# Optimization experiments

Measured on AMD Instinct MI355X. Metric: run time of the kernel, lower is better.

## Reference

```python
import jax, jax.numpy as jnp
import numpy as np

HEADS = 2

def gat_layer(x, edge_index, W, att, bias):
    # x: [N, Fin], W: [H*C, Fin], att: [1, H, 2C], bias: [C]
    N = x.shape[0]
    C = bias.shape[0]
    # add self loops (source_to_target: x_j from row 0, aggregate onto row 1)
    loop = jnp.arange(N, dtype=edge_index.dtype)
    src = jnp.concatenate([edge_index[0], loop])
    dst = jnp.concatenate([edge_index[1], loop])
    h = (x @ W.T).reshape(N, HEADS, C)          # [N, H, C]
    x_j = h[src]                                 # [E, H, C]
    x_i = h[dst]                                 # [E, H, C]
    x_cat = jnp.concatenate([x_i, x_j], axis=-1) # [E, H, 2C]
    alpha = (x_cat * att).sum(-1)                # [E, H]
    alpha = jnp.where(alpha >= 0, alpha, 0.2 * alpha)  # leaky_relu(0.2)
    # NOTE: module uses a global (not per-destination) normalization
    alpha = jnp.exp(alpha - alpha.max())
    alpha = alpha / (alpha.sum(axis=0, keepdims=True) + 1e-10)
    msg = x_j * alpha[..., None]                 # [E, H, C]
    aggr = jax.ops.segment_sum(msg, dst, num_segments=N)  # [N, H, C]
    return aggr.mean(axis=1) + bias              # [N, C]

def setup_inputs() -> dict:
    key = jax.random.key(0)
    ks = jax.random.split(key, 7)
    N, Fin, C = 50000, 128, 64
    E = 800000
    x = jax.random.normal(ks[0], (N, Fin), dtype=jnp.float32)
    edge_index = jax.random.randint(ks[1], (2, E), 0, N, dtype=jnp.int64)
    W1 = jax.random.normal(ks[2], (HEADS * C, Fin), dtype=jnp.float32) * 0.05
    att1 = jax.random.normal(ks[3], (1, HEADS, 2 * C), dtype=jnp.float32) * 0.05
    b1 = jnp.zeros((C,), dtype=jnp.float32)
    W2 = jax.random.normal(ks[4], (HEADS * C, C), dtype=jnp.float32) * 0.05
    att2 = jax.random.normal(ks[5], (1, HEADS, 2 * C), dtype=jnp.float32) * 0.05
    b2 = jnp.zeros((C,), dtype=jnp.float32)
    return {"x": x, "edge_index": edge_index, "W1": W1, "att1": att1,
            "b1": b1, "W2": W2, "att2": att2, "b2": b2}

def reference(x, edge_index, W1, att1, b1, W2, att2, b2):
    h = gat_layer(x, edge_index, W1, att1, b1)
    h = jax.nn.relu(h)
    # F.dropout with training flag: treated as eval (identity) for determinism
    out = gat_layer(h, edge_index, W2, att2, b2)
    return out
```

## Files before the change

kernel.cpp:

```cpp
#include <hip/hip_runtime.h>
#include <hip/hip_bf16.h>
#include <math.h>


#define HP 8
#define HG 64
#define NHISTB (HP * HG)
#define HRANGE_MAX 6272
#define NSELF 16
#define NWGT  256

using short8 = __attribute__((ext_vector_type(8))) short;
using f32x4  = __attribute__((ext_vector_type(4))) float;

__device__ __forceinline__ unsigned f2bf(float x) {
  unsigned u = __float_as_uint(x);
  return (u + 0x7fffu + ((u >> 16) & 1u)) >> 16;
}
__device__ __forceinline__ float bflo(unsigned p) { return __uint_as_float(p << 16); }
__device__ __forceinline__ float bfhi(unsigned p) { return __uint_as_float(p & 0xffff0000u); }
__device__ __forceinline__ float lrexp(float a) {
  a = a >= 0.f ? a : 0.2f * a;
  return __expf(a);
}

__device__ __forceinline__ void block_zadd(float z0, float z1,
                                           float* __restrict__ Zp) {
  __shared__ float r0[16], r1[16];
  int lane = threadIdx.x & 63, w = threadIdx.x >> 6;
  int nw = blockDim.x >> 6;
#pragma unroll
  for (int off = 32; off; off >>= 1) {
    z0 += __shfl_down(z0, off, 64);
    z1 += __shfl_down(z1, off, 64);
  }
  if (lane == 0) { r0[w] = z0; r1[w] = z1; }
  __syncthreads();
  if (threadIdx.x == 0) {
    float s0 = 0.f, s1 = 0.f;
    for (int i = 0; i < nw; ++i) { s0 += r0[i]; s1 += r1[i]; }
    atomicAdd(&Zp[0], s0);
    atomicAdd(&Zp[1], s1);
  }
}

__global__ __launch_bounds__(256) void init_ws(
    const float* __restrict__ W1, const float* __restrict__ W2,
    unsigned short* __restrict__ wbf1, unsigned short* __restrict__ wbf2,
    float* __restrict__ Z) {
  int tid = blockIdx.x * 256 + threadIdx.x;
  int stride = gridDim.x * 256;
  for (int i = tid; i < 128 * 128; i += stride)
    wbf1[i] = (unsigned short)f2bf(W1[i]);
  for (int i = tid; i < 128 * 64; i += stride)
    wbf2[i] = (unsigned short)f2bf(W2[i]);
  if (tid < 4) Z[tid] = 0.f;
}

template <int FIN>
__global__ __launch_bounds__(256) void gemm_mfma(
    const float* __restrict__ x, const unsigned short* __restrict__ Wb,
    const float* __restrict__ att, unsigned* __restrict__ hq,
    float* __restrict__ si, float* __restrict__ sj,
    int N,
    const int* __restrict__ dstE, unsigned short* __restrict__ partial,
    int E, int nhistb, int hstep, int eper) {
  const int tid = threadIdx.x;

  constexpr int WB = 128 * FIN * 2;
  constexpr int SMEM = (WB > HRANGE_MAX * 4) ? WB : HRANGE_MAX * 4;
  __shared__ __align__(16) unsigned char smem[SMEM];

  if ((int)blockIdx.x < nhistb) {
    int* lhist = (int*)smem;
    const int p = blockIdx.x & (HP - 1);
    const int g = blockIdx.x >> 3;
    const int lo = p * hstep;
    for (int i = tid; i < hstep; i += 256) lhist[i] = 0;
    __syncthreads();
    const int eb = g * eper;
    const int ee = min(E, eb + eper);
    int e = eb + tid;
    for (; e + 3 * 256 < ee; e += 4 * 256) {
      int d0 = dstE[e] - lo;
      int d1 = dstE[e + 256] - lo;
      int d2 = dstE[e + 2 * 256] - lo;
      int d3 = dstE[e + 3 * 256] - lo;
      if ((unsigned)d0 < (unsigned)hstep) atomicAdd(&lhist[d0], 1);
      if ((unsigned)d1 < (unsigned)hstep) atomicAdd(&lhist[d1], 1);
      if ((unsigned)d2 < (unsigned)hstep) atomicAdd(&lhist[d2], 1);
      if ((unsigned)d3 < (unsigned)hstep) atomicAdd(&lhist[d3], 1);
    }
    for (; e < ee; e += 256) {
      int d = dstE[e] - lo;
      if ((unsigned)d < (unsigned)hstep) atomicAdd(&lhist[d], 1);
    }
    __syncthreads();
    for (int i = tid; i < hstep; i += 256) {
      int node = lo + i;
      if (node < N) partial[(size_t)g * N + node] = (unsigned short)lhist[i];
    }
    return;
  }

  constexpr int KS = FIN / 32;
  constexpr int CPR = FIN / 8;
  constexpr int NCHUNK = 128 * CPR;

  unsigned short* wlds = (unsigned short*)smem;

  const int w    = tid >> 6;
  const int lane = tid & 63;
  const int cl   = lane & 15;
  const int grp  = lane >> 4;
  const int n0   = (blockIdx.x - nhistb) * 64;

  const int arow = n0 + w * 16 + cl;
  const bool avalid = arow < N;
  float4 av0[KS], av1[KS];
#pragma unroll
  for (int ks = 0; ks < KS; ++ks) {
    av0[ks] = make_float4(0.f, 0.f, 0.f, 0.f);
    av1[ks] = av0[ks];
    if (avalid) {
      const float4* xp =
          (const float4*)(x + (size_t)arow * FIN + ks * 32 + grp * 8);
      av0[ks] = xp[0];
      av1[ks] = xp[1];
    }
  }

  const uint4* Wb4 = (const uint4*)Wb;
  for (int c = tid; c < NCHUNK; c += 256) {
    int row = c / CPR;
    int cc  = c & (CPR - 1);
    *(uint4*)&wlds[row * FIN + ((cc ^ (row & (CPR - 1))) * 8)] = Wb4[c];
  }
  __syncthreads();

  short8 afrag[KS];
#pragma unroll
  for (int ks = 0; ks < KS; ++ks) {
    union { short8 s8; unsigned u[4]; } af;
    af.u[0] = f2bf(av0[ks].x) | (f2bf(av0[ks].y) << 16);
    af.u[1] = f2bf(av0[ks].z) | (f2bf(av0[ks].w) << 16);
    af.u[2] = f2bf(av1[ks].x) | (f2bf(av1[ks].y) << 16);
    af.u[3] = f2bf(av1[ks].z) | (f2bf(av1[ks].w) << 16);
    afrag[ks] = af.s8;
  }

  f32x4 acc[8];
#pragma unroll
  for (int ct = 0; ct < 8; ++ct) acc[ct] = (f32x4){0.f, 0.f, 0.f, 0.f};

  const int swz = cl & (CPR - 1);
#pragma unroll
  for (int ks = 0; ks < KS; ++ks) {
#pragma unroll
    for (int ct = 0; ct < 8; ++ct) {
      const unsigned short* bp =
          &wlds[(ct * 16 + cl) * FIN + (((ks * 4 + grp) ^ swz) * 8)];
      short8 bfrag = *(const short8*)bp;
      acc[ct] = __builtin_amdgcn_mfma_f32_16x16x32_bf16(afrag[ks], bfrag,
                                                        acc[ct], 0, 0, 0);
    }
  }

  float ai[8], aj[8];
#pragma unroll
  for (int ct = 0; ct < 8; ++ct) {
    int hd = ct >> 2;
    int cw = (ct & 3) * 16 + cl;
    ai[ct] = att[hd * 128 + cw];
    aj[ct] = att[hd * 128 + 64 + cw];
  }

#pragma unroll
  for (int r = 0; r < 4; ++r) {
    int node = n0 + w * 16 + grp * 4 + r;
    float s0i = 0.f, s0j = 0.f, s1i = 0.f, s1j = 0.f;
    unsigned wpk[4];
#pragma unroll
    for (int ct = 0; ct < 4; ++ct) {
      float v0 = acc[ct][r];
      float v1 = acc[ct + 4][r];
      s0i += v0 * ai[ct];
      s0j += v0 * aj[ct];
      s1i += v1 * ai[ct + 4];
      s1j += v1 * aj[ct + 4];
      wpk[ct] = f2bf(v0) | (f2bf(v1) << 16);
    }
#pragma unroll
    for (int off = 8; off; off >>= 1) {
      s0i += __shfl_xor(s0i, off, 64);
      s0j += __shfl_xor(s0j, off, 64);
      s1i += __shfl_xor(s1i, off, 64);
      s1j += __shfl_xor(s1j, off, 64);
    }
    if (node < N) {
#pragma unroll
      for (int ct = 0; ct < 4; ++ct)
        hq[(size_t)node * 64 + ct * 16 + cl] = wpk[ct];
      if (cl == 0) {
        si[node * 2 + 0] = s0i;
        si[node * 2 + 1] = s1i;
        sj[node * 2 + 0] = s0j;
        sj[node * 2 + 1] = s1j;
      }
    }
  }
}

__global__ __launch_bounds__(256) void scan_blocks(
    const unsigned short* __restrict__ partial, int* __restrict__ rowptr,
    int* __restrict__ bsum, int N) {
  __shared__ int ts[256];
  int b = blockIdx.x, t = threadIdx.x;
  int base = b * 1024 + t * 4;
  int s0 = 0, s1 = 0, s2 = 0, s3 = 0;
  if (base < N) {
#pragma unroll 4
    for (int g = 0; g < HG; ++g) {
      unsigned long long v =
          *(const unsigned long long*)&partial[(size_t)g * N + base];
      s0 += (int)(v & 0xffffu);
      s1 += (int)((v >> 16) & 0xffffu);
      s2 += (int)((v >> 32) & 0xffffu);
      s3 += (int)((v >> 48) & 0xffffu);
    }
  }
  int v[4] = {s0, s1, s2, s3};
  int tot = s0 + s1 + s2 + s3;
  ts[t] = tot;
  __syncthreads();
#pragma unroll
  for (int off = 1; off < 256; off <<= 1) {
    int x = (t >= off) ? ts[t - off] : 0;
    __syncthreads();
    ts[t] += x;
    __syncthreads();
  }
  int run = ts[t] - tot;
#pragma unroll
  for (int j = 0; j < 4; ++j) {
    if (base + j < N) rowptr[base + j] = run;
    run += v[j];
  }
  if (t == 255) bsum[b] = ts[255];
}

__global__ __launch_bounds__(256) void scan_finish(
    int* __restrict__ rowptr, const int* __restrict__ bsum,
    unsigned short* __restrict__ partial, int N, int Eall, int nb) {
  __shared__ int pre[256];
  if (threadIdx.x == 0) {
    int run = 0;
    for (int i = 0; i < nb; ++i) { pre[i] = run; run += bsum[i]; }
  }
  __syncthreads();
  int tid = blockIdx.x * blockDim.x + threadIdx.x;
  int stride = gridDim.x * blockDim.x;
  for (int i = tid; i < N; i += stride) {
    int v = rowptr[i] + pre[i >> 10];
    rowptr[i] = v;
    int run = 0;
#pragma unroll 8
    for (int g = 0; g < HG; ++g) {
      int c = partial[(size_t)g * N + i];
      partial[(size_t)g * N + i] = (unsigned short)run;
      run += c;
    }
  }
  if (tid == 0) rowptr[N] = Eall;
}

__global__ __launch_bounds__(1024) void scatter_z(
    const int* __restrict__ srcE, const int* __restrict__ dstE,
    const unsigned short* __restrict__ partial, const int* __restrict__ rowptr,
    float4* __restrict__ erec,
    const float2* __restrict__ si2, const float2* __restrict__ sj2,
    float* __restrict__ Zp, int E, int hstep, int N, int eper) {
  __shared__ __align__(16) int lcur[HRANGE_MAX];
  const int tid = threadIdx.x;
  float z0 = 0.f, z1 = 0.f;

  if ((int)blockIdx.x < NSELF) {
    for (int n = blockIdx.x * 1024 + tid; n < N; n += NSELF * 1024) {
      float2 a = si2[n], b = sj2[n];
      z0 += lrexp(a.x + b.x);
      z1 += lrexp(a.y + b.y);
    }
    block_zadd(z0, z1, Zp);
    return;
  }

  const int bid = blockIdx.x - NSELF;
  const int p = bid & (HP - 1);
  const int g = bid >> 3;
  const int lo = p * hstep;
  for (int i = tid; i < hstep; i += 1024) {
    int node = lo + i;
    lcur[i] = (node < N)
                  ? rowptr[node] + (int)partial[(size_t)g * N + node]
                  : 0;
  }
  __syncthreads();

  const int eb = g * eper;
  const int ee = min(E, eb + eper);
  int e = eb + tid;
  for (; e + 3 * 1024 < ee; e += 4 * 1024) {
    int d0 = dstE[e], d1 = dstE[e + 1024];
    int d2 = dstE[e + 2 * 1024], d3 = dstE[e + 3 * 1024];
    int s0 = srcE[e], s1 = srcE[e + 1024];
    int s2 = srcE[e + 2 * 1024], s3 = srcE[e + 3 * 1024];
    int t0 = d0 - lo, t1 = d1 - lo, t2 = d2 - lo, t3 = d3 - lo;
    if ((unsigned)t0 < (unsigned)hstep) {
      float2 siv = si2[d0], sjv = sj2[s0];
      float w0 = lrexp(siv.x + sjv.x), w1 = lrexp(siv.y + sjv.y);
      z0 += w0; z1 += w1;
      erec[atomicAdd(&lcur[t0], 1)] =
          make_float4(__int_as_float(s0), __int_as_float(d0), w0, w1);
    }
    if ((unsigned)t1 < (unsigned)hstep) {
      float2 siv = si2[d1], sjv = sj2[s1];
      float w0 = lrexp(siv.x + sjv.x), w1 = lrexp(siv.y + sjv.y);
      z0 += w0; z1 += w1;
      erec[atomicAdd(&lcur[t1], 1)] =
          make_float4(__int_as_float(s1), __int_as_float(d1), w0, w1);
    }
    if ((unsigned)t2 < (unsigned)hstep) {
      float2 siv = si2[d2], sjv = sj2[s2];
      float w0 = lrexp(siv.x + sjv.x), w1 = lrexp(siv.y + sjv.y);
      z0 += w0; z1 += w1;
      erec[atomicAdd(&lcur[t2], 1)] =
          make_float4(__int_as_float(s2), __int_as_float(d2), w0, w1);
    }
    if ((unsigned)t3 < (unsigned)hstep) {
      float2 siv = si2[d3], sjv = sj2[s3];
      float w0 = lrexp(siv.x + sjv.x), w1 = lrexp(siv.y + sjv.y);
      z0 += w0; z1 += w1;
      erec[atomicAdd(&lcur[t3], 1)] =
          make_float4(__int_as_float(s3), __int_as_float(d3), w0, w1);
    }
  }
  for (; e < ee; e += 1024) {
    int d = dstE[e];
    int dd = d - lo;
    if ((unsigned)dd < (unsigned)hstep) {
      int s = srcE[e];
      float2 siv = si2[d], sjv = sj2[s];
      float w0 = lrexp(siv.x + sjv.x), w1 = lrexp(siv.y + sjv.y);
      z0 += w0; z1 += w1;
      erec[atomicAdd(&lcur[dd], 1)] =
          make_float4(__int_as_float(s), __int_as_float(d), w0, w1);
    }
  }
  block_zadd(z0, z1, Zp);
}

__global__ __launch_bounds__(1024) void z_wgt2(
    const float2* __restrict__ si2, const float2* __restrict__ sj2,
    float* __restrict__ Zp, float4* __restrict__ erec, int E, int N) {
  const int tid = threadIdx.x;
  float z0 = 0.f, z1 = 0.f;
  if ((int)blockIdx.x < NSELF) {
    for (int n = blockIdx.x * 1024 + tid; n < N; n += NSELF * 1024) {
      float2 a = si2[n], b = sj2[n];
      z0 += lrexp(a.x + b.x);
      z1 += lrexp(a.y + b.y);
    }
  } else {
    int k = (blockIdx.x - NSELF) * 1024 + tid;
    for (; k < E; k += NWGT * 1024) {
      float4 r = erec[k];
      int s = __float_as_int(r.x);
      int d = __float_as_int(r.y);
      float2 siv = si2[d];
      float2 sjv = sj2[s];
      r.z = lrexp(siv.x + sjv.x);
      r.w = lrexp(siv.y + sjv.y);
      z0 += r.z; z1 += r.w;
      erec[k] = r;
    }
  }
  block_zadd(z0, z1, Zp);
}

__device__ __forceinline__ void edge8r(
    const float4* __restrict__ erec, int k, const unsigned* __restrict__ hq,
    int lane, float& acc0, float& acc1) {
  float4 r0 = erec[k],     r1 = erec[k + 1], r2 = erec[k + 2], r3 = erec[k + 3];
  float4 r4 = erec[k + 4], r5 = erec[k + 5], r6 = erec[k + 6], r7 = erec[k + 7];
  unsigned p0 = hq[(size_t)__float_as_int(r0.x) * 64 + lane];
  unsigned p1 = hq[(size_t)__float_as_int(r1.x) * 64 + lane];
  unsigned p2 = hq[(size_t)__float_as_int(r2.x) * 64 + lane];
  unsigned p3 = hq[(size_t)__float_as_int(r3.x) * 64 + lane];
  unsigned p4 = hq[(size_t)__float_as_int(r4.x) * 64 + lane];
  unsigned p5 = hq[(size_t)__float_as_int(r5.x) * 64 + lane];
  unsigned p6 = hq[(size_t)__float_as_int(r6.x) * 64 + lane];
  unsigned p7 = hq[(size_t)__float_as_int(r7.x) * 64 + lane];
  acc0 = fmaf(bflo(p0), r0.z, acc0);  acc1 = fmaf(bfhi(p0), r0.w, acc1);
  acc0 = fmaf(bflo(p1), r1.z, acc0);  acc1 = fmaf(bfhi(p1), r1.w, acc1);
  acc0 = fmaf(bflo(p2), r2.z, acc0);  acc1 = fmaf(bfhi(p2), r2.w, acc1);
  acc0 = fmaf(bflo(p3), r3.z, acc0);  acc1 = fmaf(bfhi(p3), r3.w, acc1);
  acc0 = fmaf(bflo(p4), r4.z, acc0);  acc1 = fmaf(bfhi(p4), r4.w, acc1);
  acc0 = fmaf(bflo(p5), r5.z, acc0);  acc1 = fmaf(bfhi(p5), r5.w, acc1);
  acc0 = fmaf(bflo(p6), r6.z, acc0);  acc1 = fmaf(bfhi(p6), r6.w, acc1);
  acc0 = fmaf(bflo(p7), r7.z, acc0);  acc1 = fmaf(bfhi(p7), r7.w, acc1);
}
__device__ __forceinline__ void edge4r(
    const float4* __restrict__ erec, int k, const unsigned* __restrict__ hq,
    int lane, float& acc0, float& acc1) {
  float4 r0 = erec[k], r1 = erec[k + 1], r2 = erec[k + 2], r3 = erec[k + 3];
  unsigned p0 = hq[(size_t)__float_as_int(r0.x) * 64 + lane];
  unsigned p1 = hq[(size_t)__float_as_int(r1.x) * 64 + lane];
  unsigned p2 = hq[(size_t)__float_as_int(r2.x) * 64 + lane];
  unsigned p3 = hq[(size_t)__float_as_int(r3.x) * 64 + lane];
  acc0 = fmaf(bflo(p0), r0.z, acc0);  acc1 = fmaf(bfhi(p0), r0.w, acc1);
  acc0 = fmaf(bflo(p1), r1.z, acc0);  acc1 = fmaf(bfhi(p1), r1.w, acc1);
  acc0 = fmaf(bflo(p2), r2.z, acc0);  acc1 = fmaf(bfhi(p2), r2.w, acc1);
  acc0 = fmaf(bflo(p3), r3.z, acc0);  acc1 = fmaf(bfhi(p3), r3.w, acc1);
}
__device__ __forceinline__ void edge1r(
    int s, float w0, float w1, const unsigned* __restrict__ hq, int lane,
    float& acc0, float& acc1) {
  unsigned p = hq[(size_t)s * 64 + lane];
  acc0 = fmaf(bflo(p), w0, acc0);
  acc1 = fmaf(bfhi(p), w1, acc1);
}

__global__ __launch_bounds__(256) void csr_aggregate(
    const int* __restrict__ rowptr, const float4* __restrict__ erec,
    const unsigned* __restrict__ hq, const float2* __restrict__ si2,
    const float2* __restrict__ sj2, const float* __restrict__ Zp,
    const float* __restrict__ bias, float* __restrict__ out,
    int N, int do_relu) {
  int lane = threadIdx.x & 63;
  int wid = (blockIdx.x * blockDim.x + threadIdx.x) >> 6;
  int nw = (gridDim.x * blockDim.x) >> 6;
  float z0 = 1.f / (Zp[0] + 1e-10f);
  float z1 = 1.f / (Zp[1] + 1e-10f);
  float bv = bias[lane];
  for (int n0 = wid; n0 < N; n0 += nw) {
    int n = __builtin_amdgcn_readfirstlane(n0);
    int beg = rowptr[n], end = rowptr[n + 1];
    float2 siv = si2[n];
    float2 jv = sj2[n];
    float acc0 = 0.f, acc1 = 0.f;
    edge1r(n, lrexp(siv.x + jv.x), lrexp(siv.y + jv.y), hq, lane, acc0, acc1);
    int k = beg;
    for (; k + 8 <= end; k += 8) edge8r(erec, k, hq, lane, acc0, acc1);
    if (k + 4 <= end) { edge4r(erec, k, hq, lane, acc0, acc1); k += 4; }
    for (; k < end; ++k) {
      float4 r = erec[k];
      edge1r(__float_as_int(r.x), r.z, r.w, hq, lane, acc0, acc1);
    }
    float r = 0.5f * (acc0 * z0 + acc1 * z1) + bv;
    if (do_relu) r = fmaxf(r, 0.f);
    out[(size_t)n * 64 + lane] = r;
  }
}

extern "C" void kernel_launch(void* const* d_in, const int* in_sizes, int n_in,
                              void* d_out, int out_size, void* d_ws, size_t ws_size,
                              hipStream_t stream) {
  const float* x    = (const float*)d_in[0];
  const int*   ei   = (const int*)d_in[1];
  const float* W1   = (const float*)d_in[2];
  const float* att1 = (const float*)d_in[3];
  const float* b1   = (const float*)d_in[4];
  const float* W2   = (const float*)d_in[5];
  const float* att2 = (const float*)d_in[6];
  const float* b2   = (const float*)d_in[7];
  float* out = (float*)d_out;

  const int N = in_sizes[0] / 128;
  const int E = in_sizes[1] / 2;
  const int* srcE = ei;
  const int* dstE = ei + E;

  unsigned* hq = (unsigned*)d_ws;
  float* si    = (float*)(hq + (size_t)N * 64);
  float* sj    = si + (size_t)N * 2;
  float* Z     = sj + (size_t)N * 2;
  float* x2    = Z + 4;
  unsigned short* partial = (unsigned short*)x2;
  int* rowptr  = (int*)(x2 + (size_t)N * 64);
  int* bsum    = rowptr + (N + 1);
  uintptr_t ep = ((uintptr_t)(bsum + 256) + 15) & ~(uintptr_t)15;
  float4* erec = (float4*)ep;
  unsigned short* wbf1 = (unsigned short*)(erec + E);
  unsigned short* wbf2 = wbf1 + 128 * 128;

  dim3 blk(256);
  dim3 blk1k(1024);
  int nb = (N + 1023) / 1024;
  int ntiles = (N + 63) / 64;
  int hstep = (N + HP - 1) / HP;
  int eper  = (E + HG - 1) / HG;

  init_ws<<<64, blk, 0, stream>>>(W1, W2, wbf1, wbf2, Z);
  gemm_mfma<128><<<NHISTB + ntiles, blk, 0, stream>>>(
      x, wbf1, att1, hq, si, sj, N, dstE, partial, E, NHISTB, hstep, eper);
  scan_blocks<<<nb, blk, 0, stream>>>(partial, rowptr, bsum, N);
  scan_finish<<<256, blk, 0, stream>>>(rowptr, bsum, partial, N, E, nb);
  scatter_z<<<NSELF + NHISTB, blk1k, 0, stream>>>(
      srcE, dstE, partial, rowptr, erec, (const float2*)si,
      (const float2*)sj, Z, E, hstep, N, eper);
  csr_aggregate<<<4096, blk, 0, stream>>>(rowptr, erec, hq,
                                          (const float2*)si, (const float2*)sj,
                                          Z, b1, x2, N, 1);
  gemm_mfma<64><<<ntiles, blk, 0, stream>>>(
      x2, wbf2, att2, hq, si, sj, N, dstE, partial, E, 0, hstep, eper);
  z_wgt2<<<NSELF + NWGT, blk1k, 0, stream>>>(
      (const float2*)si, (const float2*)sj, Z + 2, erec, E, N);
  csr_aggregate<<<4096, blk, 0, stream>>>(rowptr, erec, hq,
                                          (const float2*)si, (const float2*)sj,
                                          Z + 2, b2, out, N, 0);
}
```

Measured before the change: 247.9 us.

## Fuse two-pass scan into decoupled single-pass scan; store layer-1 output as bf16

Replaces the scan_blocks plus scan_finish pair with one kernel. Each block publishes its total through a flag array and spins on the flags of earlier blocks to get its prefix, and it rewrites the per-group partial offsets in the same pass. Separately, the first aggregation writes its activations as bf16, and the second GEMM loads bf16 fragments directly with no conversion. This removes a launch, a reread of partial, and half of the x2 traffic. In exchange it relies on all earlier blocks being resident for the spin-wait to make progress, and it assumes nb is at most 64 to fit the flags array.

```diff
diff --git a/kernel.cpp b/kernel.cpp
--- a/kernel.cpp
+++ b/kernel.cpp
@@ -47,7 +47,7 @@
 __global__ __launch_bounds__(256) void init_ws(
     const float* __restrict__ W1, const float* __restrict__ W2,
     unsigned short* __restrict__ wbf1, unsigned short* __restrict__ wbf2,
-    float* __restrict__ Z) {
+    float* __restrict__ Z, int* __restrict__ flags) {
   int tid = blockIdx.x * 256 + threadIdx.x;
   int stride = gridDim.x * 256;
   for (int i = tid; i < 128 * 128; i += stride)
@@ -55,11 +55,12 @@
   for (int i = tid; i < 128 * 64; i += stride)
     wbf2[i] = (unsigned short)f2bf(W2[i]);
   if (tid < 4) Z[tid] = 0.f;
-}
-
-template <int FIN>
+  if (tid < 64) flags[tid] = -1;
+}
+
+template <int FIN, bool AB16>
 __global__ __launch_bounds__(256) void gemm_mfma(
-    const float* __restrict__ x, const unsigned short* __restrict__ Wb,
+    const void* __restrict__ xin, const unsigned short* __restrict__ Wb,
     const float* __restrict__ att, unsigned* __restrict__ hq,
     float* __restrict__ si, float* __restrict__ sj,
     int N,
@@ -117,16 +118,33 @@
 
   const int arow = n0 + w * 16 + cl;
   const bool avalid = arow < N;
-  float4 av0[KS], av1[KS];
+
+  short8 afrag[KS];
 #pragma unroll
   for (int ks = 0; ks < KS; ++ks) {
-    av0[ks] = make_float4(0.f, 0.f, 0.f, 0.f);
-    av1[ks] = av0[ks];
-    if (avalid) {
-      const float4* xp =
-          (const float4*)(x + (size_t)arow * FIN + ks * 32 + grp * 8);
-      av0[ks] = xp[0];
-      av1[ks] = xp[1];
+    if constexpr (AB16) {
+      short8 z = {0, 0, 0, 0, 0, 0, 0, 0};
+      afrag[ks] = z;
+      if (avalid) {
+        const unsigned short* xb = (const unsigned short*)xin;
+        afrag[ks] =
+            *(const short8*)(xb + (size_t)arow * FIN + ks * 32 + grp * 8);
+      }
+    } else {
+      float4 v0 = make_float4(0.f, 0.f, 0.f, 0.f), v1 = v0;
+      if (avalid) {
+        const float* xf = (const float*)xin;
+        const float4* xp =
+            (const float4*)(xf + (size_t)arow * FIN + ks * 32 + grp * 8);
+        v0 = xp[0];
+        v1 = xp[1];
+      }
+      union { short8 s8; unsigned u[4]; } af;
+      af.u[0] = f2bf(v0.x) | (f2bf(v0.y) << 16);
+      af.u[1] = f2bf(v0.z) | (f2bf(v0.w) << 16);
+      af.u[2] = f2bf(v1.x) | (f2bf(v1.y) << 16);
+      af.u[3] = f2bf(v1.z) | (f2bf(v1.w) << 16);
+      afrag[ks] = af.s8;
     }
   }
 
@@ -137,17 +155,6 @@
     *(uint4*)&wlds[row * FIN + ((cc ^ (row & (CPR - 1))) * 8)] = Wb4[c];
   }
   __syncthreads();
-
-  short8 afrag[KS];
-#pragma unroll
-  for (int ks = 0; ks < KS; ++ks) {
-    union { short8 s8; unsigned u[4]; } af;
-    af.u[0] = f2bf(av0[ks].x) | (f2bf(av0[ks].y) << 16);
-    af.u[1] = f2bf(av0[ks].z) | (f2bf(av0[ks].w) << 16);
-    af.u[2] = f2bf(av1[ks].x) | (f2bf(av1[ks].y) << 16);
-    af.u[3] = f2bf(av1[ks].z) | (f2bf(av1[ks].w) << 16);
-    afrag[ks] = af.s8;
-  }
 
   f32x4 acc[8];
 #pragma unroll
@@ -211,26 +218,31 @@
   }
 }
 
-__global__ __launch_bounds__(256) void scan_blocks(
-    const unsigned short* __restrict__ partial, int* __restrict__ rowptr,
-    int* __restrict__ bsum, int N) {
+__global__ __launch_bounds__(256) void scan_full(
+    unsigned short* __restrict__ partial, int* __restrict__ rowptr,
+    int* __restrict__ flags, int N, int Eall, int nb) {
   __shared__ int ts[256];
-  int b = blockIdx.x, t = threadIdx.x;
-  int base = b * 1024 + t * 4;
-  int s0 = 0, s1 = 0, s2 = 0, s3 = 0;
+  __shared__ int pre_s;
+  const int b = blockIdx.x, t = threadIdx.x;
+  const int base = b * 1024 + t * 4;
+  int r0 = 0, r1 = 0, r2 = 0, r3 = 0;
   if (base < N) {
-#pragma unroll 4
+#pragma unroll 8
     for (int g = 0; g < HG; ++g) {
-      unsigned long long v =
-          *(const unsigned long long*)&partial[(size_t)g * N + base];
-      s0 += (int)(v & 0xffffu);
-      s1 += (int)((v >> 16) & 0xffffu);
-      s2 += (int)((v >> 32) & 0xffffu);
-      s3 += (int)((v >> 48) & 0xffffu);
-    }
-  }
-  int v[4] = {s0, s1, s2, s3};
-  int tot = s0 + s1 + s2 + s3;
+      unsigned long long* p =
+          (unsigned long long*)&partial[(size_t)g * N + base];
+      unsigned long long v = *p;
+      *p = (unsigned long long)(unsigned short)r0 |
+           ((unsigned long long)(unsigned short)r1 << 16) |
+           ((unsigned long long)(unsigned short)r2 << 32) |
+           ((unsigned long long)(unsigned short)r3 << 48);
+      r0 += (int)(v & 0xffffu);
+      r1 += (int)((v >> 16) & 0xffffu);
+      r2 += (int)((v >> 32) & 0xffffu);
+      r3 += (int)((v >> 48) & 0xffffu);
+    }
+  }
+  const int tot = r0 + r1 + r2 + r3;
   ts[t] = tot;
   __syncthreads();
 #pragma unroll
@@ -240,38 +252,35 @@
     ts[t] += x;
     __syncthreads();
   }
-  int run = ts[t] - tot;
-#pragma unroll
-  for (int j = 0; j < 4; ++j) {
-    if (base + j < N) rowptr[base + j] = run;
-    run += v[j];
-  }
-  if (t == 255) bsum[b] = ts[255];
-}
-
-__global__ __launch_bounds__(256) void scan_finish(
-    int* __restrict__ rowptr, const int* __restrict__ bsum,
-    unsigned short* __restrict__ partial, int N, int Eall, int nb) {
-  __shared__ int pre[256];
-  if (threadIdx.x == 0) {
-    int run = 0;
-    for (int i = 0; i < nb; ++i) { pre[i] = run; run += bsum[i]; }
-  }
-  __syncthreads();
-  int tid = blockIdx.x * blockDim.x + threadIdx.x;
-  int stride = gridDim.x * blockDim.x;
-  for (int i = tid; i < N; i += stride) {
-    int v = rowptr[i] + pre[i >> 10];
-    rowptr[i] = v;
-    int run = 0;
-#pragma unroll 8
-    for (int g = 0; g < HG; ++g) {
-      int c = partial[(size_t)g * N + i];
-      partial[(size_t)g * N + i] = (unsigned short)run;
-      run += c;
-    }
-  }
-  if (tid == 0) rowptr[N] = Eall;
+  const int run_local = ts[t] - tot;
+  const int blktot = ts[255];
+  if (t == 0)
+    __hip_atomic_store(&flags[b], blktot, __ATOMIC_RELEASE,
+                       __HIP_MEMORY_SCOPE_AGENT);
+  __syncthreads();
+  if (t < b) {
+    int v;
+    do {
+      v = __hip_atomic_load(&flags[t], __ATOMIC_ACQUIRE,
+                            __HIP_MEMORY_SCOPE_AGENT);
+    } while (v < 0);
+    ts[t] = v;
+  }
+  __syncthreads();
+  if (t == 0) {
+    int acc = 0;
+    for (int i = 0; i < b; ++i) acc += ts[i];
+    pre_s = acc;
+  }
+  __syncthreads();
+  int run = pre_s + run_local;
+  if (base < N) {
+    rowptr[base] = run;         run += r0;
+    rowptr[base + 1] = run;     run += r1;
+    rowptr[base + 2] = run;     run += r2;
+    rowptr[base + 3] = run;
+  }
+  if (b == nb - 1 && t == 255) rowptr[N] = Eall;
 }
 
 __global__ __launch_bounds__(1024) void scatter_z(
@@ -434,8 +443,8 @@
     const int* __restrict__ rowptr, const float4* __restrict__ erec,
     const unsigned* __restrict__ hq, const float2* __restrict__ si2,
     const float2* __restrict__ sj2, const float* __restrict__ Zp,
-    const float* __restrict__ bias, float* __restrict__ out,
-    int N, int do_relu) {
+    const float* __restrict__ bias, void* __restrict__ out,
+    int N, int do_relu, int bf16_out) {
   int lane = threadIdx.x & 63;
   int wid = (blockIdx.x * blockDim.x + threadIdx.x) >> 6;
   int nw = (gridDim.x * blockDim.x) >> 6;
@@ -458,7 +467,10 @@
     }
     float r = 0.5f * (acc0 * z0 + acc1 * z1) + bv;
     if (do_relu) r = fmaxf(r, 0.f);
-    out[(size_t)n * 64 + lane] = r;
+    if (bf16_out)
+      ((unsigned short*)out)[(size_t)n * 64 + lane] = (unsigned short)f2bf(r);
+    else
+      ((float*)out)[(size_t)n * 64 + lane] = r;
   }
 }
 
@@ -486,9 +498,10 @@
   float* Z     = sj + (size_t)N * 2;
   float* x2    = Z + 4;
   unsigned short* partial = (unsigned short*)x2;
+  unsigned short* x2b = (unsigned short*)x2;
   int* rowptr  = (int*)(x2 + (size_t)N * 64);
-  int* bsum    = rowptr + (N + 1);
-  uintptr_t ep = ((uintptr_t)(bsum + 256) + 15) & ~(uintptr_t)15;
+  int* flags   = rowptr + (N + 1);
+  uintptr_t ep = ((uintptr_t)(flags + 64) + 15) & ~(uintptr_t)15;
   float4* erec = (float4*)ep;
   unsigned short* wbf1 = (unsigned short*)(erec + E);
   unsigned short* wbf2 = wbf1 + 128 * 128;
@@ -500,22 +513,21 @@
   int hstep = (N + HP - 1) / HP;
   int eper  = (E + HG - 1) / HG;
 
-  init_ws<<<64, blk, 0, stream>>>(W1, W2, wbf1, wbf2, Z);
-  gemm_mfma<128><<<NHISTB + ntiles, blk, 0, stream>>>(
+  init_ws<<<64, blk, 0, stream>>>(W1, W2, wbf1, wbf2, Z, flags);
+  gemm_mfma<128, false><<<NHISTB + ntiles, blk, 0, stream>>>(
       x, wbf1, att1, hq, si, sj, N, dstE, partial, E, NHISTB, hstep, eper);
-  scan_blocks<<<nb, blk, 0, stream>>>(partial, rowptr, bsum, N);
-  scan_finish<<<256, blk, 0, stream>>>(rowptr, bsum, partial, N, E, nb);
+  scan_full<<<nb, blk, 0, stream>>>(partial, rowptr, flags, N, E, nb);
   scatter_z<<<NSELF + NHISTB, blk1k, 0, stream>>>(
       srcE, dstE, partial, rowptr, erec, (const float2*)si,
       (const float2*)sj, Z, E, hstep, N, eper);
   csr_aggregate<<<4096, blk, 0, stream>>>(rowptr, erec, hq,
                                           (const float2*)si, (const float2*)sj,
-                                          Z, b1, x2, N, 1);
-  gemm_mfma<64><<<ntiles, blk, 0, stream>>>(
-      x2, wbf2, att2, hq, si, sj, N, dstE, partial, E, 0, hstep, eper);
+                                          Z, b1, x2b, N, 1, 1);
+  gemm_mfma<64, true><<<ntiles, blk, 0, stream>>>(
+      x2b, wbf2, att2, hq, si, sj, N, dstE, partial, E, 0, hstep, eper);
   z_wgt2<<<NSELF + NWGT, blk1k, 0, stream>>>(
       (const float2*)si, (const float2*)sj, Z + 2, erec, E, N);
   csr_aggregate<<<4096, blk, 0, stream>>>(rowptr, erec, hq,
                                           (const float2*)si, (const float2*)sj,
-                                          Z + 2, b2, out, N, 0);
-}
+                                          Z + 2, b2, out, N, 0, 0);
+}
```

Measured after the change: 238.0 us. -4.0%, faster.
